# Kernel tuning notes

Hardware: AMD Instinct MI355X
Metric: run time of the kernel (lower is better)

Reference implementation:

```python
import jax, jax.numpy as jnp
import numpy as np


def _sobel_kernels(dtype):
    # Faithful to the torch code: each kernel has shape (1,3,3) in (kd,kh,kw),
    # i.e. a 2D Sobel applied slice-wise, but conv3d uses padding=1 on ALL dims
    # so the output depth is D+2.
    sx = np.array([[[-1, 0, 1], [-2, 0, 2], [-1, 0, 1]]], dtype=np.float32)  # (1,3,3)
    sy = np.transpose(sx, (0, 2, 1))                                          # transpose(1,2)
    sz = np.array([[[-1, -2, -1], [0, 0, 0], [1, 2, 1]]], dtype=np.float32)
    k = np.stack([sx, sy, sz])[:, None]  # (3 out, 1 in, 1, 3, 3)
    return jnp.asarray(k, dtype)


def setup_inputs() -> dict:
    key = jax.random.key(0)
    k1, k2 = jax.random.split(key)
    B, C, D, H, W = 2, 4, 96, 160, 160
    pred = jax.random.normal(k1, (B, C, D, H, W), dtype=jnp.float32)
    target = jax.random.randint(k2, (B, D, H, W), 0, C)
    return {"pred": pred, "target": target}


def reference(pred, target):
    B, C, D, H, W = pred.shape
    p = jax.nn.softmax(pred, axis=1)                                   # (B,C,D,H,W)
    t = jax.nn.one_hot(target, C, dtype=pred.dtype)                    # (B,D,H,W,C)
    t = jnp.transpose(t, (0, 4, 1, 2, 3))                              # (B,C,D,H,W)
    k = _sobel_kernels(pred.dtype)

    def sobel(x):
        # fold class into batch; 3 output channels = x/y/z gradients
        x = x.reshape(B * C, 1, D, H, W)
        return jax.lax.conv_general_dilated(
            x, k, window_strides=(1, 1, 1), padding=[(1, 1)] * 3,
            dimension_numbers=("NCDHW", "OIDHW", "NCDHW"))           # (B*C,3,D+2,H+2,W+2)

    diff = sobel(p) - sobel(t)
    # Each torch mse_loss averages over a (B,1,D+2,H+2,W+2) tensor; the 3*C
    # means are summed, then divided by num_classes.
    per_tensor = B * (D + 2) * (H + 2) * (W + 2)
    loss = jnp.sum(diff * diff) / per_tensor / C
    return loss
```

## Files before the change

### kernel.cpp

```cpp
#include <hip/hip_runtime.h>
#include <hip/hip_fp16.h>

#define NB 2
#define NC 4
#define ND 96
#define NH 160
#define NW 160

constexpr int TH    = 10;
constexpr int SR    = TH + 2;
constexpr int NBAND = NH / TH;
constexpr int NSLOT = SR * NW / 4;
constexpr int PCELL = SR * NW;
constexpr int ZCELL = PCELL;
constexpr int NBLK  = NBAND * NB * ND;
constexpr int NXCD  = 8;
constexpr int CHUNK = NBLK / NXCD;
constexpr float SCALE = 1.0f / (2.0f * 98.0f * 162.0f * 162.0f * 4.0f);

__device__ __forceinline__ __half2 ld_h2(const unsigned int* p, int i) {
    return __builtin_bit_cast(__half2, p[i]);
}

__device__ __forceinline__ void qcalc(float p0, float p1, float p2, float p3,
                                      int t, bool valid,
                                      unsigned int& ha, unsigned int& hb) {
    float q0 = 0.f, q1 = 0.f, q2 = 0.f, q3 = 0.f;
    if (valid) {
        const float m  = fmaxf(fmaxf(p0, p1), fmaxf(p2, p3));
        const float e0 = __expf(p0 - m);
        const float e1 = __expf(p1 - m);
        const float e2 = __expf(p2 - m);
        const float e3 = __expf(p3 - m);
        const float inv = 1.0f / (e0 + e1 + e2 + e3);
        q0 = e0 * inv - (t == 0 ? 1.f : 0.f);
        q1 = e1 * inv - (t == 1 ? 1.f : 0.f);
        q2 = e2 * inv - (t == 2 ? 1.f : 0.f);
        q3 = e3 * inv - (t == 3 ? 1.f : 0.f);
    }
    ha = __builtin_bit_cast(unsigned int, __floats2half2_rn(q0, q1));
    hb = __builtin_bit_cast(unsigned int, __floats2half2_rn(q2, q3));
}

__global__ __launch_bounds__(256) void boundary_loss_kernel(
    const float* __restrict__ pred,
    const int*   __restrict__ target,
    float* __restrict__ part)
{
    __shared__ unsigned int pa[PCELL + 4];
    __shared__ unsigned int pb[PCELL + 4];
    __shared__ float wsum[4];

    const int tid = threadIdx.x;

    const int lin   = blockIdx.x;
    const int lin2  = (lin & (NXCD - 1)) * CHUNK + (lin >> 3);
    const int band  = lin2 & (NBAND - 1);
    const int slice = lin2 >> 4;
    const int b     = slice / ND;
    const int d     = slice - b * ND;
    const int y0    = band * TH;

    const size_t cs4   = (size_t)ND * NH * NW / 4;
    const size_t pbase = ((size_t)b * NC * ND + d) * (size_t)(NH * NW);
    const size_t tbase = ((size_t)b * ND + d) * (size_t)(NH * NW);

    const int  rA   = tid / 40;
    const int  cA   = tid - rA * 40;
    const int  gyA  = y0 - 1 + rA;
    const bool vA   = (gyA >= 0) && (gyA < NH);
    const int  gyAc = min(max(gyA, 0), NH - 1);

    const int  sB   = tid + 256;
    const bool hasB = (sB < NSLOT);
    const int  rB   = sB / 40;
    const int  cB   = sB - rB * 40;
    const int  gyB  = y0 - 1 + rB;
    const bool vB   = hasB && (gyB >= 0) && (gyB < NH);
    const int  gyBc = min(max(gyB, 0), NH - 1);

    const float4* ppA = (const float4*)(pred + pbase + (size_t)gyAc * NW) + cA;
    const float4 a0 = ppA[0];
    const float4 a1 = ppA[cs4];
    const float4 a2 = ppA[2 * cs4];
    const float4 a3 = ppA[3 * cs4];
    const int4   ta = ((const int4*)(target + tbase + (size_t)gyAc * NW))[cA];

    const int cBs  = hasB ? cB : 0;
    const int gyBs = hasB ? gyBc : 0;
    const float4* ppB = (const float4*)(pred + pbase + (size_t)gyBs * NW) + cBs;
    const float4 b0 = ppB[0];
    const float4 b1 = ppB[cs4];
    const float4 b2 = ppB[2 * cs4];
    const float4 b3 = ppB[3 * cs4];
    const int4   tb = ((const int4*)(target + tbase + (size_t)gyBs * NW))[cBs];

    {
        uint4 wa, wb;
        qcalc(a0.x, a1.x, a2.x, a3.x, ta.x, vA, wa.x, wb.x);
        qcalc(a0.y, a1.y, a2.y, a3.y, ta.y, vA, wa.y, wb.y);
        qcalc(a0.z, a1.z, a2.z, a3.z, ta.z, vA, wa.z, wb.z);
        qcalc(a0.w, a1.w, a2.w, a3.w, ta.w, vA, wa.w, wb.w);
        ((uint4*)pa)[rA * 40 + cA] = wa;
        ((uint4*)pb)[rA * 40 + cA] = wb;
    }
    if (hasB) {
        uint4 wa, wb;
        qcalc(b0.x, b1.x, b2.x, b3.x, tb.x, vB, wa.x, wb.x);
        qcalc(b0.y, b1.y, b2.y, b3.y, tb.y, vB, wa.y, wb.y);
        qcalc(b0.z, b1.z, b2.z, b3.z, tb.z, vB, wa.z, wb.z);
        qcalc(b0.w, b1.w, b2.w, b3.w, tb.w, vB, wa.w, wb.w);
        ((uint4*)pa)[rB * 40 + cB] = wa;
        ((uint4*)pb)[rB * 40 + cB] = wb;
    }
    if (tid == 0) { pa[ZCELL] = 0u; pb[ZCELL] = 0u; }
    __syncthreads();

    float acc = 0.f;
    if (tid < NW) {
        int am = tid;
        int al = (tid > 0)      ? tid - 1 : ZCELL;
        int ar = (tid < NW - 1) ? tid + 1 : ZCELL;
        const int il = (tid > 0)      ? NW : 0;
        const int ir = (tid < NW - 1) ? NW : 0;

        const __half2 two = __floats2half2_rn(2.f, 2.f);
        const __half2 hz  = __floats2half2_rn(0.f, 0.f);
        __half2 smmA = hz, smA = hz, dmmA = hz, dmA = hz;
        __half2 smmB = hz, smB = hz, dmmB = hz, dmB = hz;

#define CLS(P, smm, sm, dmm, dm)                                          \
        do {                                                              \
            const __half2 l = ld_h2(P, al);                               \
            const __half2 m = ld_h2(P, am);                               \
            const __half2 r = ld_h2(P, ar);                               \
            const __half2 sn = __hadd2(__hfma2(m, two, l), r);            \
            const __half2 dn = __hsub2(r, l);                             \
            if (t >= 2) {                                                 \
                const __half2 gx = __hadd2(__hfma2(dm, two, dmm), dn);    \
                const __half2 gy = __hsub2(sn, smm);                      \
                const __half2 rs = __hfma2(__hmul2(gy, gy), two,          \
                                           __hmul2(gx, gx));              \
                acc += __low2float(rs) + __high2float(rs);                \
            }                                                             \
            smm = sm; sm = sn; dmm = dm; dm = dn;                         \
        } while (0)

        #pragma unroll
        for (int t = 0; t < SR; ++t) {
            CLS(pa, smmA, smA, dmmA, dmA);
            CLS(pb, smmB, smB, dmmB, dmB);
            am += NW; al += il; ar += ir;
        }
#undef CLS
    }

    #pragma unroll
    for (int off = 32; off > 0; off >>= 1)
        acc += __shfl_down(acc, off, 64);
    if ((tid & 63) == 0) wsum[tid >> 6] = acc;
    __syncthreads();
    if (tid == 0) {
        part[lin] = wsum[0] + wsum[1] + wsum[2] + wsum[3];
    }
}

__global__ __launch_bounds__(256) void reduce_partials_kernel(
    const float* __restrict__ part, float* __restrict__ out)
{
    const int tid = threadIdx.x;
    const float4* p4 = (const float4*)part;
    float s = 0.f;
    #pragma unroll
    for (int i = 0; i < NBLK / 1024; ++i) {
        const float4 v = p4[tid + i * 256];
        s += (v.x + v.y) + (v.z + v.w);
    }
    #pragma unroll
    for (int off = 32; off > 0; off >>= 1)
        s += __shfl_down(s, off, 64);
    __shared__ float wsum[4];
    if ((tid & 63) == 0) wsum[tid >> 6] = s;
    __syncthreads();
    if (tid == 0)
        out[0] = (wsum[0] + wsum[1] + wsum[2] + wsum[3]) * SCALE;
}

extern "C" void kernel_launch(void* const* d_in, const int* in_sizes, int n_in,
                              void* d_out, int out_size, void* d_ws, size_t ws_size,
                              hipStream_t stream) {
    const float* pred   = (const float*)d_in[0];
    const int*   target = (const int*)d_in[1];
    float*       out    = (float*)d_out;
    float*       part   = (float*)d_ws;

    boundary_loss_kernel<<<dim3(NBLK), 256, 0, stream>>>(pred, target, part);
    reduce_partials_kernel<<<1, 256, 0, stream>>>(part, out);
}
```

Baseline: 130.3 us.

## Process two row bands per block with ring-buffered halo reuse and prefetch

Each block now covers two consecutive 10-row bands instead of one. It reuses the two overlapping halo rows through a circular shared-memory buffer, so only 10 new rows are loaded for the second band. The global loads for the second band are issued before the first band's Sobel pass, which overlaps memory latency with compute. This cuts redundant halo loads, from 12/10 toward 11/10 rows per output, and halves the block count, at the cost of lower parallelism and an extra barrier. The reduce kernel is adjusted for the new partial count.

After: 132.6 us. No clear change (+1.7%).

```diff
diff --git a/kernel.cpp b/kernel.cpp
--- a/kernel.cpp
+++ b/kernel.cpp
@@ -9,11 +9,14 @@
 
 constexpr int TH    = 10;
 constexpr int SR    = TH + 2;
-constexpr int NBAND = NH / TH;
-constexpr int NSLOT = SR * NW / 4;
+constexpr int KIT   = 2;
+constexpr int RB    = TH * KIT;
+constexpr int NGRP  = NH / RB;
+constexpr int NBLK  = NGRP * NB * ND;
+constexpr int NSLOT0 = SR * NW / 4;
+constexpr int NSLOTR = TH * NW / 4;
 constexpr int PCELL = SR * NW;
 constexpr int ZCELL = PCELL;
-constexpr int NBLK  = NBAND * NB * ND;
 constexpr int NXCD  = 8;
 constexpr int CHUNK = NBLK / NXCD;
 constexpr float SCALE = 1.0f / (2.0f * 98.0f * 162.0f * 162.0f * 4.0f);
@@ -42,6 +45,54 @@
     hb = __builtin_bit_cast(unsigned int, __floats2half2_rn(q2, q3));
 }
 
+__device__ __forceinline__ void sobel_win(const unsigned int* pa,
+                                          const unsigned int* pb,
+                                          int tid, int base, float& acc) {
+    const bool lok = tid > 0, rok = tid < NW - 1;
+    const __half2 two = __floats2half2_rn(2.f, 2.f);
+    const __half2 hz  = __floats2half2_rn(0.f, 0.f);
+    __half2 smmA = hz, smA = hz, dmmA = hz, dmA = hz;
+    __half2 smmB = hz, smB = hz, dmmB = hz, dmB = hz;
+    int rr = base;
+    #pragma unroll
+    for (int t = 0; t < SR; ++t) {
+        const int am = rr * NW + tid;
+        const int al = lok ? am - 1 : ZCELL;
+        const int ar = rok ? am + 1 : ZCELL;
+        {
+            const __half2 l = ld_h2(pa, al);
+            const __half2 m = ld_h2(pa, am);
+            const __half2 r = ld_h2(pa, ar);
+            const __half2 sn = __hadd2(__hfma2(m, two, l), r);
+            const __half2 dn = __hsub2(r, l);
+            if (t >= 2) {
+                const __half2 gx = __hadd2(__hfma2(dmA, two, dmmA), dn);
+                const __half2 gy = __hsub2(sn, smmA);
+                const __half2 rs = __hfma2(__hmul2(gy, gy), two,
+                                           __hmul2(gx, gx));
+                acc += __low2float(rs) + __high2float(rs);
+            }
+            smmA = smA; smA = sn; dmmA = dmA; dmA = dn;
+        }
+        {
+            const __half2 l = ld_h2(pb, al);
+            const __half2 m = ld_h2(pb, am);
+            const __half2 r = ld_h2(pb, ar);
+            const __half2 sn = __hadd2(__hfma2(m, two, l), r);
+            const __half2 dn = __hsub2(r, l);
+            if (t >= 2) {
+                const __half2 gx = __hadd2(__hfma2(dmB, two, dmmB), dn);
+                const __half2 gy = __hsub2(sn, smmB);
+                const __half2 rs = __hfma2(__hmul2(gy, gy), two,
+                                           __hmul2(gx, gx));
+                acc += __low2float(rs) + __high2float(rs);
+            }
+            smmB = smB; smB = sn; dmmB = dmB; dmB = dn;
+        }
+        rr = (rr + 1 == SR) ? 0 : rr + 1;
+    }
+}
+
 __global__ __launch_bounds__(256) void boundary_loss_kernel(
     const float* __restrict__ pred,
     const int*   __restrict__ target,
@@ -55,105 +106,123 @@
 
     const int lin   = blockIdx.x;
     const int lin2  = (lin & (NXCD - 1)) * CHUNK + (lin >> 3);
-    const int band  = lin2 & (NBAND - 1);
-    const int slice = lin2 >> 4;
+    const int grp   = lin2 & (NGRP - 1);
+    const int slice = lin2 >> 3;
     const int b     = slice / ND;
     const int d     = slice - b * ND;
-    const int y0    = band * TH;
+    const int y0    = grp * RB;
 
     const size_t cs4   = (size_t)ND * NH * NW / 4;
     const size_t pbase = ((size_t)b * NC * ND + d) * (size_t)(NH * NW);
     const size_t tbase = ((size_t)b * ND + d) * (size_t)(NH * NW);
 
-    const int  rA   = tid / 40;
-    const int  cA   = tid - rA * 40;
-    const int  gyA  = y0 - 1 + rA;
-    const bool vA   = (gyA >= 0) && (gyA < NH);
-    const int  gyAc = min(max(gyA, 0), NH - 1);
-
-    const int  sB   = tid + 256;
-    const bool hasB = (sB < NSLOT);
-    const int  rB   = sB / 40;
-    const int  cB   = sB - rB * 40;
-    const int  gyB  = y0 - 1 + rB;
-    const bool vB   = hasB && (gyB >= 0) && (gyB < NH);
-    const int  gyBc = min(max(gyB, 0), NH - 1);
-
-    const float4* ppA = (const float4*)(pred + pbase + (size_t)gyAc * NW) + cA;
-    const float4 a0 = ppA[0];
-    const float4 a1 = ppA[cs4];
-    const float4 a2 = ppA[2 * cs4];
-    const float4 a3 = ppA[3 * cs4];
-    const int4   ta = ((const int4*)(target + tbase + (size_t)gyAc * NW))[cA];
-
-    const int cBs  = hasB ? cB : 0;
-    const int gyBs = hasB ? gyBc : 0;
-    const float4* ppB = (const float4*)(pred + pbase + (size_t)gyBs * NW) + cBs;
-    const float4 b0 = ppB[0];
-    const float4 b1 = ppB[cs4];
-    const float4 b2 = ppB[2 * cs4];
-    const float4 b3 = ppB[3 * cs4];
-    const int4   tb = ((const int4*)(target + tbase + (size_t)gyBs * NW))[cBs];
+    {
+        const int  rA   = tid / 40;
+        const int  cA   = tid - rA * 40;
+        const int  gyA  = y0 - 1 + rA;
+        const bool vA   = (gyA >= 0) && (gyA < NH);
+        const int  gyAc = min(max(gyA, 0), NH - 1);
+
+        const int  sB   = tid + 256;
+        const bool hasB = (sB < NSLOT0);
+        const int  rB   = sB / 40;
+        const int  cB   = sB - rB * 40;
+        const int  gyB  = y0 - 1 + rB;
+        const bool vB   = hasB && (gyB < NH);
+        const int  gyBc = min(gyB, NH - 1);
+
+        const float4* ppA = (const float4*)(pred + pbase + (size_t)gyAc * NW) + cA;
+        const float4 a0 = ppA[0];
+        const float4 a1 = ppA[cs4];
+        const float4 a2 = ppA[2 * cs4];
+        const float4 a3 = ppA[3 * cs4];
+        const int4   ta = ((const int4*)(target + tbase + (size_t)gyAc * NW))[cA];
+
+        const int cBs  = hasB ? cB : 0;
+        const int gyBs = hasB ? gyBc : 0;
+        const float4* ppB = (const float4*)(pred + pbase + (size_t)gyBs * NW) + cBs;
+        const float4 b0 = ppB[0];
+        const float4 b1 = ppB[cs4];
+        const float4 b2 = ppB[2 * cs4];
+        const float4 b3 = ppB[3 * cs4];
+        const int4   tb = ((const int4*)(target + tbase + (size_t)gyBs * NW))[cBs];
+
+        {
+            uint4 wa, wb;
+            qcalc(a0.x, a1.x, a2.x, a3.x, ta.x, vA, wa.x, wb.x);
+            qcalc(a0.y, a1.y, a2.y, a3.y, ta.y, vA, wa.y, wb.y);
+            qcalc(a0.z, a1.z, a2.z, a3.z, ta.z, vA, wa.z, wb.z);
+            qcalc(a0.w, a1.w, a2.w, a3.w, ta.w, vA, wa.w, wb.w);
+            ((uint4*)pa)[rA * 40 + cA] = wa;
+            ((uint4*)pb)[rA * 40 + cA] = wb;
+        }
+        if (hasB) {
+            uint4 wa, wb;
+            qcalc(b0.x, b1.x, b2.x, b3.x, tb.x, vB, wa.x, wb.x);
+            qcalc(b0.y, b1.y, b2.y, b3.y, tb.y, vB, wa.y, wb.y);
+            qcalc(b0.z, b1.z, b2.z, b3.z, tb.z, vB, wa.z, wb.z);
+            qcalc(b0.w, b1.w, b2.w, b3.w, tb.w, vB, wa.w, wb.w);
+            ((uint4*)pa)[rB * 40 + cB] = wa;
+            ((uint4*)pb)[rB * 40 + cB] = wb;
+        }
+    }
+    if (tid == 0) { pa[ZCELL] = 0u; pb[ZCELL] = 0u; }
+    __syncthreads();
+
+    const int  jA    = tid / 40;
+    const int  cA2   = tid - jA * 40;
+    const int  gyPA  = y0 + TH + 1 + jA;
+    const bool vPA   = gyPA < NH;
+    const int  gyPAc = min(gyPA, NH - 1);
+
+    const int  sB2   = tid + 256;
+    const bool hasB2 = (sB2 < NSLOTR);
+    const int  jB    = sB2 / 40;
+    const int  cB2   = sB2 - jB * 40;
+    const int  gyPB  = y0 + TH + 1 + jB;
+    const bool vPB   = hasB2 && (gyPB < NH);
+    const int  gyPBc = hasB2 ? min(gyPB, NH - 1) : 0;
+    const int  cB2s  = hasB2 ? cB2 : 0;
+
+    const float4* qpA = (const float4*)(pred + pbase + (size_t)gyPAc * NW) + cA2;
+    const float4 A0 = qpA[0];
+    const float4 A1 = qpA[cs4];
+    const float4 A2 = qpA[2 * cs4];
+    const float4 A3 = qpA[3 * cs4];
+    const int4   tA = ((const int4*)(target + tbase + (size_t)gyPAc * NW))[cA2];
+
+    const float4* qpB = (const float4*)(pred + pbase + (size_t)gyPBc * NW) + cB2s;
+    const float4 B0 = qpB[0];
+    const float4 B1 = qpB[cs4];
+    const float4 B2 = qpB[2 * cs4];
+    const float4 B3 = qpB[3 * cs4];
+    const int4   tB = ((const int4*)(target + tbase + (size_t)gyPBc * NW))[cB2s];
+
+    float acc = 0.f;
+    if (tid < NW) sobel_win(pa, pb, tid, 0, acc);
+    __syncthreads();
 
     {
         uint4 wa, wb;
-        qcalc(a0.x, a1.x, a2.x, a3.x, ta.x, vA, wa.x, wb.x);
-        qcalc(a0.y, a1.y, a2.y, a3.y, ta.y, vA, wa.y, wb.y);
-        qcalc(a0.z, a1.z, a2.z, a3.z, ta.z, vA, wa.z, wb.z);
-        qcalc(a0.w, a1.w, a2.w, a3.w, ta.w, vA, wa.w, wb.w);
-        ((uint4*)pa)[rA * 40 + cA] = wa;
-        ((uint4*)pb)[rA * 40 + cA] = wb;
-    }
-    if (hasB) {
+        qcalc(A0.x, A1.x, A2.x, A3.x, tA.x, vPA, wa.x, wb.x);
+        qcalc(A0.y, A1.y, A2.y, A3.y, tA.y, vPA, wa.y, wb.y);
+        qcalc(A0.z, A1.z, A2.z, A3.z, tA.z, vPA, wa.z, wb.z);
+        qcalc(A0.w, A1.w, A2.w, A3.w, tA.w, vPA, wa.w, wb.w);
+        ((uint4*)pa)[jA * 40 + cA2] = wa;
+        ((uint4*)pb)[jA * 40 + cA2] = wb;
+    }
+    if (hasB2) {
         uint4 wa, wb;
-        qcalc(b0.x, b1.x, b2.x, b3.x, tb.x, vB, wa.x, wb.x);
-        qcalc(b0.y, b1.y, b2.y, b3.y, tb.y, vB, wa.y, wb.y);
-        qcalc(b0.z, b1.z, b2.z, b3.z, tb.z, vB, wa.z, wb.z);
-        qcalc(b0.w, b1.w, b2.w, b3.w, tb.w, vB, wa.w, wb.w);
-        ((uint4*)pa)[rB * 40 + cB] = wa;
-        ((uint4*)pb)[rB * 40 + cB] = wb;
-    }
-    if (tid == 0) { pa[ZCELL] = 0u; pb[ZCELL] = 0u; }
-    __syncthreads();
-
-    float acc = 0.f;
-    if (tid < NW) {
-        int am = tid;
-        int al = (tid > 0)      ? tid - 1 : ZCELL;
-        int ar = (tid < NW - 1) ? tid + 1 : ZCELL;
-        const int il = (tid > 0)      ? NW : 0;
-        const int ir = (tid < NW - 1) ? NW : 0;
-
-        const __half2 two = __floats2half2_rn(2.f, 2.f);
-        const __half2 hz  = __floats2half2_rn(0.f, 0.f);
-        __half2 smmA = hz, smA = hz, dmmA = hz, dmA = hz;
-        __half2 smmB = hz, smB = hz, dmmB = hz, dmB = hz;
-
-#define CLS(P, smm, sm, dmm, dm)                                          \
-        do {                                                              \
-            const __half2 l = ld_h2(P, al);                               \
-            const __half2 m = ld_h2(P, am);                               \
-            const __half2 r = ld_h2(P, ar);                               \
-            const __half2 sn = __hadd2(__hfma2(m, two, l), r);            \
-            const __half2 dn = __hsub2(r, l);                             \
-            if (t >= 2) {                                                 \
-                const __half2 gx = __hadd2(__hfma2(dm, two, dmm), dn);    \
-                const __half2 gy = __hsub2(sn, smm);                      \
-                const __half2 rs = __hfma2(__hmul2(gy, gy), two,          \
-                                           __hmul2(gx, gx));              \
-                acc += __low2float(rs) + __high2float(rs);                \
-            }                                                             \
-            smm = sm; sm = sn; dmm = dm; dm = dn;                         \
-        } while (0)
-
-        #pragma unroll
-        for (int t = 0; t < SR; ++t) {
-            CLS(pa, smmA, smA, dmmA, dmA);
-            CLS(pb, smmB, smB, dmmB, dmB);
-            am += NW; al += il; ar += ir;
-        }
-#undef CLS
-    }
+        qcalc(B0.x, B1.x, B2.x, B3.x, tB.x, vPB, wa.x, wb.x);
+        qcalc(B0.y, B1.y, B2.y, B3.y, tB.y, vPB, wa.y, wb.y);
+        qcalc(B0.z, B1.z, B2.z, B3.z, tB.z, vPB, wa.z, wb.z);
+        qcalc(B0.w, B1.w, B2.w, B3.w, tB.w, vPB, wa.w, wb.w);
+        ((uint4*)pa)[jB * 40 + cB2] = wa;
+        ((uint4*)pb)[jB * 40 + cB2] = wb;
+    }
+    __syncthreads();
+
+    if (tid < NW) sobel_win(pa, pb, tid, TH, acc);
 
     #pragma unroll
     for (int off = 32; off > 0; off >>= 1)
@@ -171,9 +240,12 @@
     const int tid = threadIdx.x;
     const float4* p4 = (const float4*)part;
     float s = 0.f;
-    #pragma unroll
-    for (int i = 0; i < NBLK / 1024; ++i) {
-        const float4 v = p4[tid + i * 256];
+    {
+        const float4 v = p4[tid];
+        s += (v.x + v.y) + (v.z + v.w);
+    }
+    if (tid < NBLK / 4 - 256) {
+        const float4 v = p4[256 + tid];
         s += (v.x + v.y) + (v.z + v.w);
     }
     #pragma unroll
```

## Replace LDS tile with per-wave register stencil using lane shuffles and double-buffered loads

Applied to the files above, without the earlier changes.

Each wavefront now handles one overlapping column strip of a 10-row band. Horizontal neighbours come from lane shuffles instead of a shared-memory tile, and the next row's loads are software-pipelined into a double buffer. The change removes the LDS staging, the block-level barriers and the idle threads of the old compute phase, so all lanes work on the stencil. In exchange, about two halo columns per strip are computed twice, loads shrink from float4 to float2, and the number of partial sums grows.

New measurement: 133.5 us. +2.5%, slower.

```diff
diff --git a/kernel.cpp b/kernel.cpp
--- a/kernel.cpp
+++ b/kernel.cpp
@@ -7,24 +7,21 @@
 #define NH 160
 #define NW 160
 
-constexpr int TH    = 10;
-constexpr int SR    = TH + 2;
-constexpr int NBAND = NH / TH;
-constexpr int NSLOT = SR * NW / 4;
-constexpr int PCELL = SR * NW;
-constexpr int ZCELL = PCELL;
-constexpr int NBLK  = NBAND * NB * ND;
-constexpr int NXCD  = 8;
-constexpr int CHUNK = NBLK / NXCD;
+constexpr int ROWS   = 10;
+constexpr int NBANDV = NH / ROWS;
+constexpr int NSTRIP = 2;
+constexpr int NTASK  = NSTRIP * NBANDV * NB * ND;
+constexpr int NBLK   = NTASK / 4;
 constexpr float SCALE = 1.0f / (2.0f * 98.0f * 162.0f * 162.0f * 4.0f);
 
-__device__ __forceinline__ __half2 ld_h2(const unsigned int* p, int i) {
-    return __builtin_bit_cast(__half2, p[i]);
-}
-
-__device__ __forceinline__ void qcalc(float p0, float p1, float p2, float p3,
-                                      int t, bool valid,
-                                      unsigned int& ha, unsigned int& hb) {
+__device__ __forceinline__ __half2 shfl_h2(__half2 v, int src) {
+    return __builtin_bit_cast(
+        __half2, __shfl(__builtin_bit_cast(unsigned int, v), src, 64));
+}
+
+__device__ __forceinline__ void qcalc2(float p0, float p1, float p2, float p3,
+                                       int t, bool valid,
+                                       __half2& qa, __half2& qb) {
     float q0 = 0.f, q1 = 0.f, q2 = 0.f, q3 = 0.f;
     if (valid) {
         const float m  = fmaxf(fmaxf(p0, p1), fmaxf(p2, p3));
@@ -38,8 +35,8 @@
         q2 = e2 * inv - (t == 2 ? 1.f : 0.f);
         q3 = e3 * inv - (t == 3 ? 1.f : 0.f);
     }
-    ha = __builtin_bit_cast(unsigned int, __floats2half2_rn(q0, q1));
-    hb = __builtin_bit_cast(unsigned int, __floats2half2_rn(q2, q3));
+    qa = __floats2half2_rn(q0, q1);
+    qb = __floats2half2_rn(q2, q3);
 }
 
 __global__ __launch_bounds__(256) void boundary_loss_kernel(
@@ -47,122 +44,129 @@
     const int*   __restrict__ target,
     float* __restrict__ part)
 {
-    __shared__ unsigned int pa[PCELL + 4];
-    __shared__ unsigned int pb[PCELL + 4];
-    __shared__ float wsum[4];
-
-    const int tid = threadIdx.x;
-
-    const int lin   = blockIdx.x;
-    const int lin2  = (lin & (NXCD - 1)) * CHUNK + (lin >> 3);
-    const int band  = lin2 & (NBAND - 1);
-    const int slice = lin2 >> 4;
+    const int tid  = threadIdx.x;
+    const int lane = tid & 63;
+    const int task = blockIdx.x * 4 + (tid >> 6);
+    const int strip = task & 1;
+    const int band  = (task >> 1) & (NBANDV - 1);
+    const int slice = task >> 5;
     const int b     = slice / ND;
     const int d     = slice - b * ND;
-    const int y0    = band * TH;
-
-    const size_t cs4   = (size_t)ND * NH * NW / 4;
-    const size_t pbase = ((size_t)b * NC * ND + d) * (size_t)(NH * NW);
-    const size_t tbase = ((size_t)b * ND + d) * (size_t)(NH * NW);
-
-    const int  rA   = tid / 40;
-    const int  cA   = tid - rA * 40;
-    const int  gyA  = y0 - 1 + rA;
-    const bool vA   = (gyA >= 0) && (gyA < NH);
-    const int  gyAc = min(max(gyA, 0), NH - 1);
-
-    const int  sB   = tid + 256;
-    const bool hasB = (sB < NSLOT);
-    const int  rB   = sB / 40;
-    const int  cB   = sB - rB * 40;
-    const int  gyB  = y0 - 1 + rB;
-    const bool vB   = hasB && (gyB >= 0) && (gyB < NH);
-    const int  gyBc = min(max(gyB, 0), NH - 1);
-
-    const float4* ppA = (const float4*)(pred + pbase + (size_t)gyAc * NW) + cA;
-    const float4 a0 = ppA[0];
-    const float4 a1 = ppA[cs4];
-    const float4 a2 = ppA[2 * cs4];
-    const float4 a3 = ppA[3 * cs4];
-    const int4   ta = ((const int4*)(target + tbase + (size_t)gyAc * NW))[cA];
-
-    const int cBs  = hasB ? cB : 0;
-    const int gyBs = hasB ? gyBc : 0;
-    const float4* ppB = (const float4*)(pred + pbase + (size_t)gyBs * NW) + cBs;
-    const float4 b0 = ppB[0];
-    const float4 b1 = ppB[cs4];
-    const float4 b2 = ppB[2 * cs4];
-    const float4 b3 = ppB[3 * cs4];
-    const int4   tb = ((const int4*)(target + tbase + (size_t)gyBs * NW))[cBs];
-
-    {
-        uint4 wa, wb;
-        qcalc(a0.x, a1.x, a2.x, a3.x, ta.x, vA, wa.x, wb.x);
-        qcalc(a0.y, a1.y, a2.y, a3.y, ta.y, vA, wa.y, wb.y);
-        qcalc(a0.z, a1.z, a2.z, a3.z, ta.z, vA, wa.z, wb.z);
-        qcalc(a0.w, a1.w, a2.w, a3.w, ta.w, vA, wa.w, wb.w);
-        ((uint4*)pa)[rA * 40 + cA] = wa;
-        ((uint4*)pb)[rA * 40 + cA] = wb;
+    const int y0    = band * ROWS;
+
+    const int  ce = strip * 126 + 2 * lane;
+    const int  cc = min(ce, NW - 2);
+    const bool vE = ce < NW;
+    const bool vO = (ce + 1) < NW;
+    const int  outLo = strip ? 127 : 0;
+    const int  outHi = strip ? 159 : 126;
+    const bool oE = (ce >= outLo) && (ce <= outHi);
+    const bool oO = (ce + 1 >= outLo) && (ce + 1 <= outHi);
+
+    const size_t plane = (size_t)NH * NW;
+    const float* pc0 = pred + ((size_t)(b * NC + 0) * ND + d) * plane;
+    const float* pc1 = pred + ((size_t)(b * NC + 1) * ND + d) * plane;
+    const float* pc2 = pred + ((size_t)(b * NC + 2) * ND + d) * plane;
+    const float* pc3 = pred + ((size_t)(b * NC + 3) * ND + d) * plane;
+    const int*   tg0 = target + ((size_t)b * ND + d) * plane;
+
+    const int upL = (lane == 0)  ? 0  : lane - 1;
+    const int dnL = (lane == 63) ? 63 : lane + 1;
+    const bool killL = (strip == 0) && (lane == 0);
+
+    const __half2 two = __floats2half2_rn(2.f, 2.f);
+    const __half2 hz  = __floats2half2_rn(0.f, 0.f);
+
+    __half2 sAe2 = hz, sAe1 = hz, dAe2 = hz, dAe1 = hz;
+    __half2 sAo2 = hz, sAo1 = hz, dAo2 = hz, dAo1 = hz;
+    __half2 sBe2 = hz, sBe1 = hz, dBe2 = hz, dBe1 = hz;
+    __half2 sBo2 = hz, sBo1 = hz, dBo2 = hz, dBo1 = hz;
+    float accE = 0.f, accO = 0.f;
+
+    float2 L0[2], L1[2], L2[2], L3[2]; int2 LT[2];
+
+    auto issue = [&](int t, int buf) {
+        const int y  = y0 - 1 + t;
+        const int yc = min(max(y, 0), NH - 1);
+        const size_t ro = (size_t)yc * NW + cc;
+        L0[buf] = *(const float2*)(pc0 + ro);
+        L1[buf] = *(const float2*)(pc1 + ro);
+        L2[buf] = *(const float2*)(pc2 + ro);
+        L3[buf] = *(const float2*)(pc3 + ro);
+        LT[buf] = *(const int2*)(tg0 + ro);
+    };
+
+    issue(0, 0);
+    #pragma unroll
+    for (int t = 0; t < ROWS + 2; ++t) {
+        const int cur = t & 1;
+        if (t + 1 < ROWS + 2) issue(t + 1, cur ^ 1);
+
+        const int  y  = y0 - 1 + t;
+        const bool vy = (y >= 0) && (y < NH);
+
+        __half2 qaE, qbE, qaO, qbO;
+        qcalc2(L0[cur].x, L1[cur].x, L2[cur].x, L3[cur].x, LT[cur].x,
+               vy && vE, qaE, qbE);
+        qcalc2(L0[cur].y, L1[cur].y, L2[cur].y, L3[cur].y, LT[cur].y,
+               vy && vO, qaO, qbO);
+
+        __half2 qaU = shfl_h2(qaO, upL); if (killL) qaU = hz;
+        __half2 qbU = shfl_h2(qbO, upL); if (killL) qbU = hz;
+        __half2 qaD = shfl_h2(qaE, dnL);
+        __half2 qbD = shfl_h2(qbE, dnL);
+
+        const __half2 sAe = __hadd2(__hfma2(qaE, two, qaU), qaO);
+        const __half2 dAe = __hsub2(qaO, qaU);
+        const __half2 sAo = __hadd2(__hfma2(qaO, two, qaE), qaD);
+        const __half2 dAo = __hsub2(qaD, qaE);
+        const __half2 sBe = __hadd2(__hfma2(qbE, two, qbU), qbO);
+        const __half2 dBe = __hsub2(qbO, qbU);
+        const __half2 sBo = __hadd2(__hfma2(qbO, two, qbE), qbD);
+        const __half2 dBo = __hsub2(qbD, qbE);
+
+        if (t >= 2) {
+            {
+                const __half2 gx = __hadd2(__hfma2(dAe1, two, dAe2), dAe);
+                const __half2 gy = __hsub2(sAe, sAe2);
+                const __half2 rs = __hfma2(__hmul2(gy, gy), two,
+                                           __hmul2(gx, gx));
+                accE += __low2float(rs) + __high2float(rs);
+            }
+            {
+                const __half2 gx = __hadd2(__hfma2(dBe1, two, dBe2), dBe);
+                const __half2 gy = __hsub2(sBe, sBe2);
+                const __half2 rs = __hfma2(__hmul2(gy, gy), two,
+                                           __hmul2(gx, gx));
+                accE += __low2float(rs) + __high2float(rs);
+            }
+            {
+                const __half2 gx = __hadd2(__hfma2(dAo1, two, dAo2), dAo);
+                const __half2 gy = __hsub2(sAo, sAo2);
+                const __half2 rs = __hfma2(__hmul2(gy, gy), two,
+                                           __hmul2(gx, gx));
+                accO += __low2float(rs) + __high2float(rs);
+            }
+            {
+                const __half2 gx = __hadd2(__hfma2(dBo1, two, dBo2), dBo);
+                const __half2 gy = __hsub2(sBo, sBo2);
+                const __half2 rs = __hfma2(__hmul2(gy, gy), two,
+                                           __hmul2(gx, gx));
+                accO += __low2float(rs) + __high2float(rs);
+            }
+        }
+        sAe2 = sAe1; sAe1 = sAe; dAe2 = dAe1; dAe1 = dAe;
+        sAo2 = sAo1; sAo1 = sAo; dAo2 = dAo1; dAo1 = dAo;
+        sBe2 = sBe1; sBe1 = sBe; dBe2 = dBe1; dBe1 = dBe;
+        sBo2 = sBo1; sBo1 = sBo; dBo2 = dBo1; dBo1 = dBo;
     }
-    if (hasB) {
-        uint4 wa, wb;
-        qcalc(b0.x, b1.x, b2.x, b3.x, tb.x, vB, wa.x, wb.x);
-        qcalc(b0.y, b1.y, b2.y, b3.y, tb.y, vB, wa.y, wb.y);
-        qcalc(b0.z, b1.z, b2.z, b3.z, tb.z, vB, wa.z, wb.z);
-        qcalc(b0.w, b1.w, b2.w, b3.w, tb.w, vB, wa.w, wb.w);
-        ((uint4*)pa)[rB * 40 + cB] = wa;
-        ((uint4*)pb)[rB * 40 + cB] = wb;
-    }
-    if (tid == 0) { pa[ZCELL] = 0u; pb[ZCELL] = 0u; }
-    __syncthreads();
-
-    float acc = 0.f;
-    if (tid < NW) {
-        int am = tid;
-        int al = (tid > 0)      ? tid - 1 : ZCELL;
-        int ar = (tid < NW - 1) ? tid + 1 : ZCELL;
-        const int il = (tid > 0)      ? NW : 0;
-        const int ir = (tid < NW - 1) ? NW : 0;
-
-        const __half2 two = __floats2half2_rn(2.f, 2.f);
-        const __half2 hz  = __floats2half2_rn(0.f, 0.f);
-        __half2 smmA = hz, smA = hz, dmmA = hz, dmA = hz;
-        __half2 smmB = hz, smB = hz, dmmB = hz, dmB = hz;
-
-#define CLS(P, smm, sm, dmm, dm)                                          \
-        do {                                                              \
-            const __half2 l = ld_h2(P, al);                               \
-            const __half2 m = ld_h2(P, am);                               \
-            const __half2 r = ld_h2(P, ar);                               \
-            const __half2 sn = __hadd2(__hfma2(m, two, l), r);            \
-            const __half2 dn = __hsub2(r, l);                             \
-            if (t >= 2) {                                                 \
-                const __half2 gx = __hadd2(__hfma2(dm, two, dmm), dn);    \
-                const __half2 gy = __hsub2(sn, smm);                      \
-                const __half2 rs = __hfma2(__hmul2(gy, gy), two,          \
-                                           __hmul2(gx, gx));              \
-                acc += __low2float(rs) + __high2float(rs);                \
-            }                                                             \
-            smm = sm; sm = sn; dmm = dm; dm = dn;                         \
-        } while (0)
-
-        #pragma unroll
-        for (int t = 0; t < SR; ++t) {
-            CLS(pa, smmA, smA, dmmA, dmA);
-            CLS(pb, smmB, smB, dmmB, dmB);
-            am += NW; al += il; ar += ir;
-        }
-#undef CLS
-    }
+
+    float acc = (oE ? accE : 0.f) + (oO ? accO : 0.f);
 
     #pragma unroll
     for (int off = 32; off > 0; off >>= 1)
         acc += __shfl_down(acc, off, 64);
-    if ((tid & 63) == 0) wsum[tid >> 6] = acc;
-    __syncthreads();
-    if (tid == 0) {
-        part[lin] = wsum[0] + wsum[1] + wsum[2] + wsum[3];
-    }
+    if (lane == 0) part[task] = acc;
 }
 
 __global__ __launch_bounds__(256) void reduce_partials_kernel(
@@ -172,7 +176,7 @@
     const float4* p4 = (const float4*)part;
     float s = 0.f;
     #pragma unroll
-    for (int i = 0; i < NBLK / 1024; ++i) {
+    for (int i = 0; i < NTASK / 1024; ++i) {
         const float4 v = p4[tid + i * 256];
         s += (v.x + v.y) + (v.z + v.w);
     }
```
